# Kernel tuning notes

Hardware: AMD Instinct MI355X
Metric: run time of the kernel (lower is better)

The kernel has to match this reference:

```python
import jax, jax.numpy as jnp
import numpy as np

B, S, H, NH = 2, 2048, 1024, 16
HD = H // NH  # head_dim = 64
ROPE_BASE = 10000.0


def _rope(x):
    # x: [B, NH, S, HD]; LLaMA-style half-split rotary embedding
    s, d = x.shape[2], x.shape[3]
    inv_freq = 1.0 / (ROPE_BASE ** (jnp.arange(0, d, 2, dtype=jnp.float32) / d))  # [d/2]
    ang = jnp.arange(s, dtype=jnp.float32)[:, None] * inv_freq[None, :]            # [S, d/2]
    cos, sin = jnp.cos(ang), jnp.sin(ang)
    x1, x2 = x[..., : d // 2], x[..., d // 2:]
    return jnp.concatenate([x1 * cos - x2 * sin, x1 * sin + x2 * cos], axis=-1)


def setup_inputs() -> dict:
    key = jax.random.key(0)
    ks = jax.random.split(key, 9)
    hidden_states = jax.random.normal(ks[0], (B, S, H), dtype=jnp.float32)
    # causal mask: True = attend
    causal = jnp.tril(jnp.ones((S, S), dtype=bool))
    attention_mask = jnp.broadcast_to(causal[None, None, :, :], (B, 1, S, S))
    std = 0.02
    wq = jax.random.normal(ks[1], (H, NH * HD), dtype=jnp.float32) * std
    wk = jax.random.normal(ks[2], (H, NH * HD), dtype=jnp.float32) * std
    wv = jax.random.normal(ks[3], (H, NH * HD), dtype=jnp.float32) * std
    wo = jax.random.normal(ks[4], (NH * HD, H), dtype=jnp.float32) * std
    bq = jnp.zeros((NH * HD,), dtype=jnp.float32)
    bk = jnp.zeros((NH * HD,), dtype=jnp.float32)
    bv = jnp.zeros((NH * HD,), dtype=jnp.float32)
    bo = jnp.zeros((H,), dtype=jnp.float32)
    return {"hidden_states": hidden_states, "attention_mask": attention_mask,
            "wq": wq, "bq": bq, "wk": wk, "bk": bk, "wv": wv, "bv": bv,
            "wo": wo, "bo": bo}


def _split_heads(x):
    b, s, _ = x.shape
    return jnp.transpose(x.reshape(b, s, NH, HD), (0, 2, 1, 3))


def reference(hidden_states, attention_mask, wq, bq, wk, bk, wv, bv, wo, bo):
    q = _split_heads(hidden_states @ wq + bq)  # [B,NH,S,HD]
    k = _split_heads(hidden_states @ wk + bk)
    v = _split_heads(hidden_states @ wv + bv)
    q = _rope(q)
    k = _rope(k)
    scores = jnp.einsum('bhqd,bhkd->bhqk', q, k) / jnp.sqrt(jnp.float32(HD))
    scores = jnp.where(attention_mask, scores, jnp.float32(-1e9))
    weights = jax.nn.softmax(scores, axis=-1)
    attn = jnp.einsum('bhqk,bhkv->bhqv', weights, v)  # [B,NH,S,HD]
    attn = jnp.transpose(attn, (0, 2, 1, 3)).reshape(hidden_states.shape[0], attn.shape[2], H)
    return attn @ wo + bo
```

## Files before the change

kernel.cpp:

```cpp
#include <hip/hip_runtime.h>
#include <math.h>

typedef short bf16x8 __attribute__((ext_vector_type(8)));
typedef float f32x4  __attribute__((ext_vector_type(4)));

__device__ __forceinline__ unsigned short f2bf(float f) {
    union { float f; unsigned u; } v; v.f = f;
    unsigned r = v.u + 0x7FFFu + ((v.u >> 16) & 1u);
    return (unsigned short)(r >> 16);
}

#define GLDS16(gp, lp) __builtin_amdgcn_global_load_lds( \
    (const __attribute__((address_space(1))) void*)(gp), \
    (__attribute__((address_space(3))) void*)(lp), 16, 0, 0)

__global__ __launch_bounds__(256)
void cvt_x(const float* __restrict__ X, unsigned short* __restrict__ Xb)
{
    const size_t t = (size_t)blockIdx.x * 256 + threadIdx.x;
    const float4 a = *(const float4*)(X + t * 8);
    const float4 b = *(const float4*)(X + t * 8 + 4);
    unsigned short u[8] = { f2bf(a.x), f2bf(a.y), f2bf(a.z), f2bf(a.w),
                            f2bf(b.x), f2bf(b.y), f2bf(b.z), f2bf(b.w) };
    *(int4*)(Xb + t * 8) = *(int4*)u;
}

__global__ __launch_bounds__(256)
void transpose_w(const float* __restrict__ w0, const float* __restrict__ w1,
                 const float* __restrict__ w2, const float* __restrict__ w3,
                 unsigned short* o0, unsigned short* o1,
                 unsigned short* o2, unsigned short* o3)
{
    const float* W; unsigned short* O;
    switch (blockIdx.z) {
        case 0: W = w0; O = o0; break;
        case 1: W = w1; O = o1; break;
        case 2: W = w2; O = o2; break;
        default: W = w3; O = o3; break;
    }
    __shared__ float T[64][65];
    const int tid = threadIdx.x;
    const int n0 = blockIdx.x * 64, k0 = blockIdx.y * 64;
    #pragma unroll
    for (int i = 0; i < 4; i++) {
        const int k = (tid >> 4) + i * 16, n4 = (tid & 15) * 4;
        const float4 v = *(const float4*)(W + (size_t)(k0 + k) * 1024 + n0 + n4);
        T[k][n4] = v.x; T[k][n4+1] = v.y; T[k][n4+2] = v.z; T[k][n4+3] = v.w;
    }
    __syncthreads();
    #pragma unroll
    for (int i = 0; i < 4; i++) {
        const int n = (tid >> 4) + i * 16, k4 = (tid & 15) * 4;
        unsigned short u[4] = { f2bf(T[k4][n]), f2bf(T[k4+1][n]),
                                f2bf(T[k4+2][n]), f2bf(T[k4+3][n]) };
        *(int2*)(O + (size_t)(n0 + n) * 1024 + k0 + k4) = *(int2*)u;
    }
}

__global__ __launch_bounds__(256)
void transpose_v(const unsigned short* __restrict__ Vb, unsigned short* __restrict__ Vtb)
{
    __shared__ unsigned short T[64][72];
    const int tid = threadIdx.x, bh = blockIdx.y, s0 = blockIdx.x * 64;
    const size_t base = (size_t)bh * 2048 * 64;
    #pragma unroll
    for (int i = 0; i < 2; i++) {
        const int s = (tid >> 3) + i * 32, d8 = (tid & 7) * 8;
        *(int4*)&T[s][d8] = *(const int4*)(Vb + base + (size_t)(s0 + s) * 64 + d8);
    }
    __syncthreads();
    #pragma unroll
    for (int i = 0; i < 2; i++) {
        const int d = (tid >> 3) + i * 32, s8 = (tid & 7) * 8;
        unsigned short u[8];
        #pragma unroll
        for (int j = 0; j < 8; j++) u[j] = T[s8 + j][d];
        *(int4*)(Vtb + base + (size_t)d * 2048 + s0 + s8) = *(int4*)u;
    }
}

__global__ __launch_bounds__(256)
void qkv_gemm(const unsigned short* __restrict__ Xb,
              const unsigned short* __restrict__ Wtq, const unsigned short* __restrict__ Wtk,
              const unsigned short* __restrict__ Wtv,
              const float* __restrict__ bq, const float* __restrict__ bk,
              const float* __restrict__ bv,
              unsigned short* __restrict__ Qb, unsigned short* __restrict__ Kb,
              unsigned short* __restrict__ Vb)
{
    const unsigned short* Wt; const float* bias; unsigned short* Out;
    const int z = blockIdx.z;
    if (z == 0)      { Wt = Wtq; bias = bq; Out = Qb; }
    else if (z == 1) { Wt = Wtk; bias = bk; Out = Kb; }
    else             { Wt = Wtv; bias = bv; Out = Vb; }

    __shared__ unsigned short As[128 * 32];
    __shared__ unsigned short Bs[128 * 32];
    const int tid = threadIdx.x, lane = tid & 63, w = tid >> 6;
    const int quad = lane >> 4, c = lane & 15;
    const int wr = w >> 1, wc = w & 1;
    const int m0 = blockIdx.x * 128, n0 = blockIdx.y * 128;

    const int srow = lane >> 2, scol = (lane & 3) * 8;

    f32x4 acc[4][4];
    #pragma unroll
    for (int i = 0; i < 4; i++)
        #pragma unroll
        for (int j = 0; j < 4; j++) acc[i][j] = (f32x4){0.f, 0.f, 0.f, 0.f};

    for (int k0 = 0; k0 < 1024; k0 += 32) {
        #pragma unroll
        for (int j = 0; j < 2; j++) {
            const int r = w * 32 + j * 16;
            GLDS16(Xb + (size_t)(m0 + r + srow) * 1024 + k0 + scol, &As[r * 32]);
            GLDS16(Wt + (size_t)(n0 + r + srow) * 1024 + k0 + scol, &Bs[r * 32]);
        }
        __syncthreads();
        bf16x8 af[4], bf[4];
        #pragma unroll
        for (int rt = 0; rt < 4; rt++)
            af[rt] = *(const bf16x8*)&As[(wr * 64 + rt * 16 + c) * 32 + quad * 8];
        #pragma unroll
        for (int nt = 0; nt < 4; nt++)
            bf[nt] = *(const bf16x8*)&Bs[(wc * 64 + nt * 16 + c) * 32 + quad * 8];
        #pragma unroll
        for (int rt = 0; rt < 4; rt++)
            #pragma unroll
            for (int nt = 0; nt < 4; nt++)
                acc[rt][nt] = __builtin_amdgcn_mfma_f32_16x16x32_bf16(af[rt], bf[nt], acc[rt][nt], 0, 0, 0);
        __syncthreads();
    }

    const int h = (n0 + wc * 64) >> 6;
    const bool rope = (z < 2);
    const float kLn = 9.210340371976184f / 32.0f;
    const float inv0 = expf(-(float)c * kLn);
    const float inv1 = expf(-(float)(c + 16) * kLn);
    float bv4[4];
    #pragma unroll
    for (int nt = 0; nt < 4; nt++) bv4[nt] = bias[n0 + wc * 64 + nt * 16 + c];

    #pragma unroll
    for (int rt = 0; rt < 4; rt++) {
        #pragma unroll
        for (int reg = 0; reg < 4; reg++) {
            const int m = m0 + wr * 64 + rt * 16 + quad * 4 + reg;
            const int b = m >> 11, s = m & 2047;
            float x0 = acc[rt][0][reg] + bv4[0];
            float x1 = acc[rt][1][reg] + bv4[1];
            float x2 = acc[rt][2][reg] + bv4[2];
            float x3 = acc[rt][3][reg] + bv4[3];
            float y0 = x0, y1 = x1, y2 = x2, y3 = x3;
            if (rope) {
                float sn0, cs0, sn1, cs1;
                sincosf((float)s * inv0, &sn0, &cs0);
                sincosf((float)s * inv1, &sn1, &cs1);
                y0 = x0 * cs0 - x2 * sn0;  y2 = x0 * sn0 + x2 * cs0;
                y1 = x1 * cs1 - x3 * sn1;  y3 = x1 * sn1 + x3 * cs1;
            }
            unsigned short* dst = Out + ((size_t)(b * 16 + h) * 2048 + s) * 64;
            dst[0 * 16 + c] = f2bf(y0);
            dst[1 * 16 + c] = f2bf(y1);
            dst[2 * 16 + c] = f2bf(y2);
            dst[3 * 16 + c] = f2bf(y3);
        }
    }
}

__global__ __launch_bounds__(256)
void out_gemm(const unsigned short* __restrict__ Ab, const unsigned short* __restrict__ Wto,
              const float* __restrict__ bo, float* __restrict__ Out)
{
    __shared__ unsigned short As[128 * 32];
    __shared__ unsigned short Bs[128 * 32];
    const int tid = threadIdx.x, lane = tid & 63, w = tid >> 6;
    const int quad = lane >> 4, c = lane & 15;
    const int wr = w >> 1, wc = w & 1;
    const int m0 = blockIdx.x * 128, n0 = blockIdx.y * 128;
    const int srow = lane >> 2, scol = (lane & 3) * 8;

    f32x4 acc[4][4];
    #pragma unroll
    for (int i = 0; i < 4; i++)
        #pragma unroll
        for (int j = 0; j < 4; j++) acc[i][j] = (f32x4){0.f, 0.f, 0.f, 0.f};

    for (int k0 = 0; k0 < 1024; k0 += 32) {
        #pragma unroll
        for (int j = 0; j < 2; j++) {
            const int r = w * 32 + j * 16;
            GLDS16(Ab  + (size_t)(m0 + r + srow) * 1024 + k0 + scol, &As[r * 32]);
            GLDS16(Wto + (size_t)(n0 + r + srow) * 1024 + k0 + scol, &Bs[r * 32]);
        }
        __syncthreads();
        bf16x8 af[4], bf[4];
        #pragma unroll
        for (int rt = 0; rt < 4; rt++)
            af[rt] = *(const bf16x8*)&As[(wr * 64 + rt * 16 + c) * 32 + quad * 8];
        #pragma unroll
        for (int nt = 0; nt < 4; nt++)
            bf[nt] = *(const bf16x8*)&Bs[(wc * 64 + nt * 16 + c) * 32 + quad * 8];
        #pragma unroll
        for (int rt = 0; rt < 4; rt++)
            #pragma unroll
            for (int nt = 0; nt < 4; nt++)
                acc[rt][nt] = __builtin_amdgcn_mfma_f32_16x16x32_bf16(af[rt], bf[nt], acc[rt][nt], 0, 0, 0);
        __syncthreads();
    }
    #pragma unroll
    for (int rt = 0; rt < 4; rt++) {
        #pragma unroll
        for (int reg = 0; reg < 4; reg++) {
            const int m = m0 + wr * 64 + rt * 16 + quad * 4 + reg;
            #pragma unroll
            for (int nt = 0; nt < 4; nt++) {
                const int n = n0 + wc * 64 + nt * 16 + c;
                Out[(size_t)m * 1024 + n] = acc[rt][nt][reg] + bo[n];
            }
        }
    }
}

__global__ __launch_bounds__(256)
void attn_part(const unsigned short* __restrict__ Qb, const unsigned short* __restrict__ Kb,
               const unsigned short* __restrict__ Vtb, unsigned short* __restrict__ Ab,
               float* __restrict__ Opart, float* __restrict__ Lpart)
{
    __shared__ unsigned short Ks[64 * 72];
    __shared__ unsigned short Vs[65 * 72];
    __shared__ unsigned short Ps[4 * 16 * 72];

    const int tid = threadIdx.x, w = tid >> 6, lane = tid & 63;
    const int quad = lane >> 4, c = lane & 15;
    const int bh = blockIdx.y;
    const int x = (blockIdx.x < 32) ? (int)blockIdx.x + 16 : (int)blockIdx.x - 32;
    int i, start, len;
    if (x < 32) { i = x + 1;  start = 0;  len = (i < 16) ? i : 16; }
    else        { i = x - 15; start = 16; len = i - 16; }
    const int q0 = (i - 1) * 64;
    const bool complete = (start == 0) && (len == i);
    const size_t base = (size_t)bh * 2048 * 64;

    if (tid < 64) Vs[64 * 72 + tid] = 0x3F80;

    const int qbase = q0 + w * 16;
    const int qrow  = qbase + c;
    const size_t qoff = base + (size_t)qrow * 64;
    const bf16x8 qf0 = *(const bf16x8*)(Qb + qoff + quad * 8);
    const bf16x8 qf1 = *(const bf16x8*)(Qb + qoff + 32 + quad * 8);

    f32x4 O[4], Osum;
    Osum = (f32x4){0.f, 0.f, 0.f, 0.f};
    #pragma unroll
    for (int nt = 0; nt < 4; nt++) O[nt] = (f32x4){0.f, 0.f, 0.f, 0.f};

    const int r0s = tid >> 3, r1s = r0s + 32, c8 = (tid & 7) * 8;

    int k0 = start * 64;
    int4 kreg0 = *(const int4*)(Kb  + base + (size_t)(k0 + r0s) * 64 + c8);
    int4 kreg1 = *(const int4*)(Kb  + base + (size_t)(k0 + r1s) * 64 + c8);
    int4 vreg0 = *(const int4*)(Vtb + base + (size_t)r0s * 2048 + k0 + c8);
    int4 vreg1 = *(const int4*)(Vtb + base + (size_t)r1s * 2048 + k0 + c8);

    unsigned short* Pw = Ps + w * 16 * 72;

    for (int t = 0; t < len; t++, k0 += 64) {
        *(int4*)&Ks[(size_t)r0s * 72 + c8] = kreg0;
        *(int4*)&Ks[(size_t)r1s * 72 + c8] = kreg1;
        *(int4*)&Vs[(size_t)r0s * 72 + c8] = vreg0;
        *(int4*)&Vs[(size_t)r1s * 72 + c8] = vreg1;
        __syncthreads();

        if (t + 1 < len) {
            const int kn = k0 + 64;
            kreg0 = *(const int4*)(Kb  + base + (size_t)(kn + r0s) * 64 + c8);
            kreg1 = *(const int4*)(Kb  + base + (size_t)(kn + r1s) * 64 + c8);
            vreg0 = *(const int4*)(Vtb + base + (size_t)r0s * 2048 + kn + c8);
            vreg1 = *(const int4*)(Vtb + base + (size_t)r1s * 2048 + kn + c8);
        }

        const bool need_mask = (k0 + 63) > qbase;

        #pragma unroll
        for (int nt = 0; nt < 4; nt++) {
            const bf16x8 kf0 = *(const bf16x8*)&Ks[(nt * 16 + c) * 72 + quad * 8];
            const bf16x8 kf1 = *(const bf16x8*)&Ks[(nt * 16 + c) * 72 + 32 + quad * 8];
            f32x4 s4 = (f32x4){0.f, 0.f, 0.f, 0.f};
            s4 = __builtin_amdgcn_mfma_f32_16x16x32_bf16(kf0, qf0, s4, 0, 0, 0);
            s4 = __builtin_amdgcn_mfma_f32_16x16x32_bf16(kf1, qf1, s4, 0, 0, 0);
            const int keyb = k0 + nt * 16 + quad * 4;
            unsigned short u[4];
            #pragma unroll
            for (int reg = 0; reg < 4; reg++) {
                float p = __expf(s4[reg] * 0.125f);
                if (need_mask && (keyb + reg > qrow)) p = 0.f;
                u[reg] = f2bf(p);
            }
            *(int2*)&Pw[c * 72 + nt * 16 + quad * 4] = *(int2*)u;
        }

        const bf16x8 pa0 = *(const bf16x8*)&Pw[c * 72 + quad * 8];
        const bf16x8 pa1 = *(const bf16x8*)&Pw[c * 72 + 32 + quad * 8];
        #pragma unroll
        for (int nt = 0; nt < 4; nt++) {
            const bf16x8 vb0 = *(const bf16x8*)&Vs[(nt * 16 + c) * 72 + quad * 8];
            const bf16x8 vb1 = *(const bf16x8*)&Vs[(nt * 16 + c) * 72 + 32 + quad * 8];
            O[nt] = __builtin_amdgcn_mfma_f32_16x16x32_bf16(pa0, vb0, O[nt], 0, 0, 0);
            O[nt] = __builtin_amdgcn_mfma_f32_16x16x32_bf16(pa1, vb1, O[nt], 0, 0, 0);
        }
        const bf16x8 on0 = *(const bf16x8*)&Vs[64 * 72 + quad * 8];
        const bf16x8 on1 = *(const bf16x8*)&Vs[64 * 72 + 32 + quad * 8];
        Osum = __builtin_amdgcn_mfma_f32_16x16x32_bf16(pa0, on0, Osum, 0, 0, 0);
        Osum = __builtin_amdgcn_mfma_f32_16x16x32_bf16(pa1, on1, Osum, 0, 0, 0);
        __syncthreads();
    }

    if (complete) {
        const int b = bh >> 4, h = bh & 15;
        #pragma unroll
        for (int reg = 0; reg < 4; reg++) {
            const float inv = 1.0f / Osum[reg];
            const int q = qbase + quad * 4 + reg;
            const size_t rowoff = ((size_t)(b * 2048 + q)) * 1024 + h * 64;
            #pragma unroll
            for (int nt = 0; nt < 4; nt++)
                Ab[rowoff + nt * 16 + c] = f2bf(O[nt][reg] * inv);
        }
    } else {
        const int pslot = (i - 17) * 2 + (start ? 1 : 0);
        float* Op = Opart + ((size_t)bh * 32 + pslot) * 4096;
        float* Lp = Lpart + ((size_t)bh * 32 + pslot) * 64;
        #pragma unroll
        for (int reg = 0; reg < 4; reg++) {
            const int row = w * 16 + quad * 4 + reg;
            #pragma unroll
            for (int nt = 0; nt < 4; nt++)
                Op[(size_t)row * 64 + nt * 16 + c] = O[nt][reg];
            if (c == 0) Lp[row] = Osum[reg];
        }
    }
}

__global__ __launch_bounds__(256)
void attn_combine(const float* __restrict__ Opart, const float* __restrict__ Lpart,
                  unsigned short* __restrict__ Ab)
{
    const int tid = threadIdx.x;
    const int j = blockIdx.x, bh = blockIdx.y;
    const int q0 = (j + 16) * 64;
    const size_t s0 = ((size_t)bh * 32 + j * 2) * 4096;
    const size_t l0 = ((size_t)bh * 32 + j * 2) * 64;

    __shared__ float linv[64];
    if (tid < 64) linv[tid] = 1.0f / (Lpart[l0 + tid] + Lpart[l0 + 64 + tid]);
    __syncthreads();

    const int row = tid >> 2, col0 = (tid & 3) * 16;
    const float inv = linv[row];
    const int b = bh >> 4, h = bh & 15;
    const int q = q0 + row;
    unsigned short* dst = Ab + ((size_t)(b * 2048 + q)) * 1024 + h * 64 + col0;
    #pragma unroll
    for (int c4 = 0; c4 < 16; c4 += 4) {
        const float4 a  = *(const float4*)(Opart + s0 + (size_t)row * 64 + col0 + c4);
        const float4 bb = *(const float4*)(Opart + s0 + 4096 + (size_t)row * 64 + col0 + c4);
        dst[c4 + 0] = f2bf((a.x + bb.x) * inv);
        dst[c4 + 1] = f2bf((a.y + bb.y) * inv);
        dst[c4 + 2] = f2bf((a.z + bb.z) * inv);
        dst[c4 + 3] = f2bf((a.w + bb.w) * inv);
    }
}

extern "C" void kernel_launch(void* const* d_in, const int* in_sizes, int n_in,
                              void* d_out, int out_size, void* d_ws, size_t ws_size,
                              hipStream_t stream)
{
    const float* X  = (const float*)d_in[0];
    const float* wq = (const float*)d_in[2];
    const float* bq = (const float*)d_in[3];
    const float* wk = (const float*)d_in[4];
    const float* bk = (const float*)d_in[5];
    const float* wv = (const float*)d_in[6];
    const float* bv = (const float*)d_in[7];
    const float* wo = (const float*)d_in[8];
    const float* bo = (const float*)d_in[9];

    unsigned short* ws = (unsigned short*)d_ws;
    const size_t M1 = 1024 * 1024;
    unsigned short* Xb  = ws;
    unsigned short* Wtq = Xb  + 4 * M1;
    unsigned short* Wtk = Wtq + M1;
    unsigned short* Wtv = Wtk + M1;
    unsigned short* Wto = Wtv + M1;
    unsigned short* Qb  = Wto + M1;
    unsigned short* Kb  = Qb  + 4 * M1;
    unsigned short* Vb  = Kb  + 4 * M1;
    unsigned short* Vtb = Vb  + 4 * M1;
    unsigned short* Ab  = Vtb + 4 * M1;
    float* Opart = (float*)(Ab + 4 * M1);
    float* Lpart = Opart + (size_t)32 * 32 * 4096;

    cvt_x       <<<2048, 256, 0, stream>>>(X, Xb);
    transpose_w <<<dim3(16, 16, 4), 256, 0, stream>>>(wq, wk, wv, wo, Wtq, Wtk, Wtv, Wto);
    qkv_gemm    <<<dim3(32, 8, 3), 256, 0, stream>>>(Xb, Wtq, Wtk, Wtv, bq, bk, bv, Qb, Kb, Vb);
    transpose_v <<<dim3(32, 32), 256, 0, stream>>>(Vb, Vtb);
    attn_part   <<<dim3(48, 32), 256, 0, stream>>>(Qb, Kb, Vtb, Ab, Opart, Lpart);
    attn_combine<<<dim3(16, 32), 256, 0, stream>>>(Opart, Lpart, Ab);
    out_gemm    <<<dim3(32, 8), 256, 0, stream>>>(Ab, Wto, bo, (float*)d_out);
}
```

Measured before the change: 231.8 us.

## Vectorize head-dim stores via permuted layout and double-buffer K/V tiles in attention

Q/K/V outputs and attention outputs are stored with a permuted head-dim order so each lane writes four contiguous bf16 values in one vector store instead of four scattered scalar stores. The permutation is undone by pre-permuting the rows of the output projection weight during its transpose, so Wo's reduction order matches the new layout. Attention partial outputs are stored as float4 in the same permuted order, so attn_combine must agree with it. Separately, K/V shared tiles are double-buffered, which removes the trailing barrier per iteration at the cost of doubled LDS usage.

```diff
diff --git a/kernel.cpp b/kernel.cpp
--- a/kernel.cpp
+++ b/kernel.cpp
@@ -13,6 +13,7 @@
 #define GLDS16(gp, lp) __builtin_amdgcn_global_load_lds( \
     (const __attribute__((address_space(1))) void*)(gp), \
     (__attribute__((address_space(3))) void*)(lp), 16, 0, 0)
+
 
 __global__ __launch_bounds__(256)
 void cvt_x(const float* __restrict__ X, unsigned short* __restrict__ Xb)
@@ -48,12 +49,28 @@
         T[k][n4] = v.x; T[k][n4+1] = v.y; T[k][n4+2] = v.z; T[k][n4+3] = v.w;
     }
     __syncthreads();
-    #pragma unroll
-    for (int i = 0; i < 4; i++) {
-        const int n = (tid >> 4) + i * 16, k4 = (tid & 15) * 4;
-        unsigned short u[4] = { f2bf(T[k4][n]), f2bf(T[k4+1][n]),
-                                f2bf(T[k4+2][n]), f2bf(T[k4+3][n]) };
-        *(int2*)(O + (size_t)(n0 + n) * 1024 + k0 + k4) = *(int2*)u;
+    if (blockIdx.z == 3) {
+        #pragma unroll
+        for (int i = 0; i < 4; i++) {
+            const int n = (tid >> 4) + i * 16, k4 = (tid & 15) * 4;
+            unsigned short u[4];
+            #pragma unroll
+            for (int j = 0; j < 4; j++) {
+                const int q = k4 + j;
+                const int p = (q & 3) * 16 + (q >> 2);
+                const int d = (p & 3) * 16 + (p >> 2);
+                u[j] = f2bf(T[d][n]);
+            }
+            *(int2*)(O + (size_t)(n0 + n) * 1024 + k0 + k4) = *(int2*)u;
+        }
+    } else {
+        #pragma unroll
+        for (int i = 0; i < 4; i++) {
+            const int n = (tid >> 4) + i * 16, k4 = (tid & 15) * 4;
+            unsigned short u[4] = { f2bf(T[k4][n]), f2bf(T[k4+1][n]),
+                                    f2bf(T[k4+2][n]), f2bf(T[k4+3][n]) };
+            *(int2*)(O + (size_t)(n0 + n) * 1024 + k0 + k4) = *(int2*)u;
+        }
     }
 }
 
@@ -100,7 +117,6 @@
     const int quad = lane >> 4, c = lane & 15;
     const int wr = w >> 1, wc = w & 1;
     const int m0 = blockIdx.x * 128, n0 = blockIdx.y * 128;
-
     const int srow = lane >> 2, scol = (lane & 3) * 8;
 
     f32x4 acc[4][4];
@@ -159,11 +175,9 @@
                 y0 = x0 * cs0 - x2 * sn0;  y2 = x0 * sn0 + x2 * cs0;
                 y1 = x1 * cs1 - x3 * sn1;  y3 = x1 * sn1 + x3 * cs1;
             }
+            unsigned short u[4] = { f2bf(y0), f2bf(y1), f2bf(y2), f2bf(y3) };
             unsigned short* dst = Out + ((size_t)(b * 16 + h) * 2048 + s) * 64;
-            dst[0 * 16 + c] = f2bf(y0);
-            dst[1 * 16 + c] = f2bf(y1);
-            dst[2 * 16 + c] = f2bf(y2);
-            dst[3 * 16 + c] = f2bf(y3);
+            *(int2*)(dst + c * 4) = *(int2*)u;
         }
     }
 }
@@ -227,8 +241,8 @@
                const unsigned short* __restrict__ Vtb, unsigned short* __restrict__ Ab,
                float* __restrict__ Opart, float* __restrict__ Lpart)
 {
-    __shared__ unsigned short Ks[64 * 72];
-    __shared__ unsigned short Vs[65 * 72];
+    __shared__ unsigned short Ks[2][64 * 72];
+    __shared__ unsigned short Vs[2][65 * 72];
     __shared__ unsigned short Ps[4 * 16 * 72];
 
     const int tid = threadIdx.x, w = tid >> 6, lane = tid & 63;
@@ -242,7 +256,7 @@
     const bool complete = (start == 0) && (len == i);
     const size_t base = (size_t)bh * 2048 * 64;
 
-    if (tid < 64) Vs[64 * 72 + tid] = 0x3F80;
+    if (tid < 64) { Vs[0][64 * 72 + tid] = 0x3F80; Vs[1][64 * 72 + tid] = 0x3F80; }
 
     const int qbase = q0 + w * 16;
     const int qrow  = qbase + c;
@@ -264,12 +278,15 @@
     int4 vreg1 = *(const int4*)(Vtb + base + (size_t)r1s * 2048 + k0 + c8);
 
     unsigned short* Pw = Ps + w * 16 * 72;
+    int cur = 0;
 
     for (int t = 0; t < len; t++, k0 += 64) {
-        *(int4*)&Ks[(size_t)r0s * 72 + c8] = kreg0;
-        *(int4*)&Ks[(size_t)r1s * 72 + c8] = kreg1;
-        *(int4*)&Vs[(size_t)r0s * 72 + c8] = vreg0;
-        *(int4*)&Vs[(size_t)r1s * 72 + c8] = vreg1;
+        unsigned short* Kc = Ks[cur];
+        unsigned short* Vc = Vs[cur];
+        *(int4*)&Kc[(size_t)r0s * 72 + c8] = kreg0;
+        *(int4*)&Kc[(size_t)r1s * 72 + c8] = kreg1;
+        *(int4*)&Vc[(size_t)r0s * 72 + c8] = vreg0;
+        *(int4*)&Vc[(size_t)r1s * 72 + c8] = vreg1;
         __syncthreads();
 
         if (t + 1 < len) {
@@ -284,8 +301,8 @@
 
         #pragma unroll
         for (int nt = 0; nt < 4; nt++) {
-            const bf16x8 kf0 = *(const bf16x8*)&Ks[(nt * 16 + c) * 72 + quad * 8];
-            const bf16x8 kf1 = *(const bf16x8*)&Ks[(nt * 16 + c) * 72 + 32 + quad * 8];
+            const bf16x8 kf0 = *(const bf16x8*)&Kc[(nt * 16 + c) * 72 + quad * 8];
+            const bf16x8 kf1 = *(const bf16x8*)&Kc[(nt * 16 + c) * 72 + 32 + quad * 8];
             f32x4 s4 = (f32x4){0.f, 0.f, 0.f, 0.f};
             s4 = __builtin_amdgcn_mfma_f32_16x16x32_bf16(kf0, qf0, s4, 0, 0, 0);
             s4 = __builtin_amdgcn_mfma_f32_16x16x32_bf16(kf1, qf1, s4, 0, 0, 0);
@@ -304,16 +321,16 @@
         const bf16x8 pa1 = *(const bf16x8*)&Pw[c * 72 + 32 + quad * 8];
         #pragma unroll
         for (int nt = 0; nt < 4; nt++) {
-            const bf16x8 vb0 = *(const bf16x8*)&Vs[(nt * 16 + c) * 72 + quad * 8];
-            const bf16x8 vb1 = *(const bf16x8*)&Vs[(nt * 16 + c) * 72 + 32 + quad * 8];
+            const bf16x8 vb0 = *(const bf16x8*)&Vc[(nt * 16 + c) * 72 + quad * 8];
+            const bf16x8 vb1 = *(const bf16x8*)&Vc[(nt * 16 + c) * 72 + 32 + quad * 8];
             O[nt] = __builtin_amdgcn_mfma_f32_16x16x32_bf16(pa0, vb0, O[nt], 0, 0, 0);
             O[nt] = __builtin_amdgcn_mfma_f32_16x16x32_bf16(pa1, vb1, O[nt], 0, 0, 0);
         }
-        const bf16x8 on0 = *(const bf16x8*)&Vs[64 * 72 + quad * 8];
-        const bf16x8 on1 = *(const bf16x8*)&Vs[64 * 72 + 32 + quad * 8];
+        const bf16x8 on0 = *(const bf16x8*)&Vc[64 * 72 + quad * 8];
+        const bf16x8 on1 = *(const bf16x8*)&Vc[64 * 72 + 32 + quad * 8];
         Osum = __builtin_amdgcn_mfma_f32_16x16x32_bf16(pa0, on0, Osum, 0, 0, 0);
         Osum = __builtin_amdgcn_mfma_f32_16x16x32_bf16(pa1, on1, Osum, 0, 0, 0);
-        __syncthreads();
+        cur ^= 1;
     }
 
     if (complete) {
@@ -322,10 +339,11 @@
         for (int reg = 0; reg < 4; reg++) {
             const float inv = 1.0f / Osum[reg];
             const int q = qbase + quad * 4 + reg;
-            const size_t rowoff = ((size_t)(b * 2048 + q)) * 1024 + h * 64;
-            #pragma unroll
-            for (int nt = 0; nt < 4; nt++)
-                Ab[rowoff + nt * 16 + c] = f2bf(O[nt][reg] * inv);
+            unsigned short u[4];
+            #pragma unroll
+            for (int nt = 0; nt < 4; nt++) u[nt] = f2bf(O[nt][reg] * inv);
+            unsigned short* dst = Ab + ((size_t)(b * 2048 + q)) * 1024 + h * 64;
+            *(int2*)(dst + c * 4) = *(int2*)u;
         }
     } else {
         const int pslot = (i - 17) * 2 + (start ? 1 : 0);
@@ -334,9 +352,8 @@
         #pragma unroll
         for (int reg = 0; reg < 4; reg++) {
             const int row = w * 16 + quad * 4 + reg;
-            #pragma unroll
-            for (int nt = 0; nt < 4; nt++)
-                Op[(size_t)row * 64 + nt * 16 + c] = O[nt][reg];
+            float4 o4 = make_float4(O[0][reg], O[1][reg], O[2][reg], O[3][reg]);
+            *(float4*)(Op + (size_t)row * 64 + c * 4) = o4;
             if (c == 0) Lp[row] = Osum[reg];
         }
     }
```

Measured after the change: 231.1 us. No clear change (-0.3%).
